# Kernel optimization log

Measured on AMD Instinct MI355X. Metric: run time of the kernel, lower is better.

Reference implementation:

```python
import jax, jax.numpy as jnp
import numpy as np

N = 50000      # nodes
E = 800000     # edges (avg degree 16)
D_IN, D_H, D_OUT = 128, 256, 128


def setup_inputs() -> dict:
    key = jax.random.key(0)
    ks = jax.random.split(key, 12)
    x = jax.random.normal(ks[0], (N, D_IN), jnp.float32)
    src = jax.random.randint(ks[1], (E,), 0, N)
    dst = jax.random.randint(ks[2], (E,), 0, N)

    def lin(k, din, dout):
        return (jax.random.normal(k, (din, dout), jnp.float32) / np.sqrt(din)).astype(jnp.float32)

    dims = [(D_IN, D_H), (D_H, D_H), (D_H, D_OUT)]
    params = {}
    ki = 3
    for i, (di, do) in enumerate(dims):
        params[f"W_self{i}"] = lin(ks[ki], di, do); ki += 1
        params[f"W_neigh{i}"] = lin(ks[ki], di, do); ki += 1
        params[f"b{i}"] = jnp.zeros((do,), jnp.float32)
    return {"x": x, "src": src, "dst": dst, **params}


def _mean_agg(h, src, dst):
    # gather src features along edges, segment-mean into dst nodes
    msg = jnp.take(h, src, axis=0)                              # [E, D]
    s = jax.ops.segment_sum(msg, dst, num_segments=N)           # [N, D]
    deg = jax.ops.segment_sum(jnp.ones((dst.shape[0], 1), h.dtype), dst, num_segments=N)
    return s / jnp.maximum(deg, 1.0)                            # zero-degree -> 0, as in DGL


def reference(x, src, dst,
              W_self0, W_neigh0, b0,
              W_self1, W_neigh1, b1,
              W_self2, W_neigh2, b2):
    Ws = [(W_self0, W_neigh0, b0), (W_self1, W_neigh1, b1), (W_self2, W_neigh2, b2)]
    h = x
    for i, (Ws_i, Wn_i, b_i) in enumerate(Ws):
        neigh = _mean_agg(h, src, dst)
        h = h @ Ws_i + neigh @ Wn_i + b_i                       # SAGEConv('mean')
        if i < len(Ws) - 1:
            h = jax.nn.relu(h)                                  # activation between layers
    return h
```

## Files before the change

### kernel.cpp

```cpp
#include <hip/hip_runtime.h>

#define NN 50000
#define NE 800000
#define NCHK 200
#define CHKE 4000
#define NBUK 196
#define BCAP 5120
#define NOFF (NBUK * NCHK)
#define NSB  ((NOFF + 255) / 256)

typedef __attribute__((ext_vector_type(8))) short short8;
typedef __attribute__((ext_vector_type(4))) float f32x4;
typedef unsigned int u32;
typedef unsigned short u16;

__device__ __forceinline__ float bf2f(short u) {
    union { unsigned int i; float f; } c;
    c.i = ((unsigned int)(unsigned short)u) << 16;
    return c.f;
}
__device__ __forceinline__ short f2bf(float f) {
    union { float f; unsigned int i; } c; c.f = f;
    unsigned int u = c.i;
    unsigned int r = (u + 0x7FFFu + ((u >> 16) & 1u)) >> 16;
    return (short)r;
}


__global__ void cvt_f32_bf16_kernel(const float* __restrict__ in, short* __restrict__ out, int n) {
    int gid = blockIdx.x * 256 + threadIdx.x;
    if (gid < n) out[gid] = f2bf(in[gid]);
}

__global__ void wcvt_all_kernel(const float* __restrict__ Ws0, const float* __restrict__ Wn0,
                                const float* __restrict__ Ws1, const float* __restrict__ Wn1,
                                const float* __restrict__ Ws2, const float* __restrict__ Wn2,
                                short* __restrict__ wts) {
    int gid = blockIdx.x * 256 + threadIdx.x;
    const float* W; int K, Dout, base, loc;
    if (gid < 65536)       { K = 128; Dout = 256; base = (gid < 32768)  ? 0 : 32768;
                             W = (gid < 32768)  ? Ws0 : Wn0; loc = gid & 32767; }
    else if (gid < 196608) { K = 256; Dout = 256; base = (gid < 131072) ? 65536 : 131072;
                             W = (gid < 131072) ? Ws1 : Wn1; loc = (gid - 65536) & 65535; }
    else                   { K = 256; Dout = 128; base = (gid < 229376) ? 196608 : 229376;
                             W = (gid < 229376) ? Ws2 : Wn2; loc = (gid - 196608) & 32767; }
    int k = loc / Dout, d = loc - k * Dout;
    int kt = k >> 6, ks = (k >> 5) & 1, kg = (k >> 3) & 3, j = k & 7;
    int cgp = d >> 4, l = d & 15;
    int off = ((((kt * 2 + ks) * (Dout >> 4) + cgp) * 4 + kg) * 16 + l) * 8 + j;
    wts[base + off] = f2bf(W[(long)k * Dout + d]);
}

__global__ __launch_bounds__(256) void bucket_hist_kernel(const int* __restrict__ dst,
                                                          int* __restrict__ chist) {
    __shared__ int lh[NBUK];
    int b = blockIdx.x, t = threadIdx.x;
    for (int i = t; i < NBUK; i += 256) lh[i] = 0;
    __syncthreads();
    int base = b * CHKE;
    for (int i = t; i < CHKE; i += 256) atomicAdd(&lh[dst[base + i] >> 8], 1);
    __syncthreads();
    for (int i = t; i < NBUK; i += 256) chist[i * NCHK + b] = lh[i];
}

__global__ __launch_bounds__(256) void off_blocksum_kernel(const int* __restrict__ in,
                                                           int* __restrict__ bsum) {
    __shared__ int sm[256];
    int t = threadIdx.x;
    int idx = blockIdx.x * 256 + t;
    sm[t] = (idx < NOFF) ? in[idx] : 0;
    __syncthreads();
    for (int off = 128; off > 0; off >>= 1) {
        if (t < off) sm[t] += sm[t + off];
        __syncthreads();
    }
    if (t == 0) bsum[blockIdx.x] = sm[0];
}

__global__ __launch_bounds__(256) void off_scanb_kernel(const int* __restrict__ bsum,
                                                        int* __restrict__ bpre) {
    __shared__ int sm[256];
    int t = threadIdx.x;
    sm[t] = (t < NSB) ? bsum[t] : 0;
    __syncthreads();
    for (int o = 1; o < 256; o <<= 1) {
        int v = sm[t];
        int a = (t >= o) ? sm[t - o] : 0;
        __syncthreads();
        sm[t] = v + a;
        __syncthreads();
    }
    if (t < NSB) bpre[t] = (t == 0) ? 0 : sm[t - 1];
}

__global__ __launch_bounds__(256) void off_scatter_kernel(const int* __restrict__ in,
                                                          const int* __restrict__ bpre,
                                                          int* __restrict__ off) {
    __shared__ int sm[256];
    int t = threadIdx.x;
    int idx = blockIdx.x * 256 + t;
    int val = (idx < NOFF) ? in[idx] : 0;
    sm[t] = val;
    __syncthreads();
    for (int o = 1; o < 256; o <<= 1) {
        int v = sm[t];
        int a = (t >= o) ? sm[t - o] : 0;
        __syncthreads();
        sm[t] = v + a;
        __syncthreads();
    }
    if (idx < NOFF) off[idx] = bpre[blockIdx.x] + sm[t] - val;
}

__global__ __launch_bounds__(256) void bucket_scatter_kernel(const int* __restrict__ src,
                                                             const int* __restrict__ dst,
                                                             const int* __restrict__ off,
                                                             u32* __restrict__ ebuf) {
    __shared__ int lcur[NBUK];
    int b = blockIdx.x, t = threadIdx.x;
    for (int i = t; i < NBUK; i += 256) lcur[i] = off[i * NCHK + b];
    __syncthreads();
    int base = b * CHKE;
    for (int i = t; i < CHKE; i += 256) {
        int d = dst[base + i], s = src[base + i];
        int slot = atomicAdd(&lcur[d >> 8], 1);
        ebuf[slot] = ((u32)(d & 255) << 16) | (u32)s;
    }
}

__global__ __launch_bounds__(256) void bucket_sort_kernel(const u32* __restrict__ ebuf,
                                                          const int* __restrict__ off,
                                                          u16* __restrict__ srcs16,
                                                          int* __restrict__ row_start,
                                                          int* __restrict__ cnt) {
    __shared__ u32 earr[BCAP];
    __shared__ u16 s16[BCAP];
    __shared__ int lhist[256], lpre[256], lcur[256];
    int k = blockIdx.x, t = threadIdx.x;
    int base = off[k * NCHK];
    int end  = (k < NBUK - 1) ? off[(k + 1) * NCHK] : NE;
    int nE = end - base;
    lhist[t] = 0;
    __syncthreads();
    for (int i = t; i < nE; i += 256) {
        u32 e = ebuf[base + i];
        earr[i] = e;
        atomicAdd(&lhist[e >> 16], 1);
    }
    __syncthreads();
    int v = lhist[t];
    lpre[t] = v;
    __syncthreads();
    for (int o = 1; o < 256; o <<= 1) {
        int x = lpre[t];
        int a = (t >= o) ? lpre[t - o] : 0;
        __syncthreads();
        lpre[t] = x + a;
        __syncthreads();
    }
    int excl = lpre[t] - v;
    int node = k * 256 + t;
    if (node < NN) { row_start[node] = base + excl; cnt[node] = v; }
    lcur[t] = excl;
    __syncthreads();
    for (int i = t; i < nE; i += 256) {
        u32 e = earr[i];
        int pos = atomicAdd(&lcur[e >> 16], 1);
        s16[pos] = (u16)(e & 0xFFFFu);
    }
    __syncthreads();
    for (int i = t; i < nE; i += 256) srcs16[base + i] = s16[i];
}

template<int NOUT, int KK, int GD, bool SAGE, bool RELU, bool OUT_F32>
__global__ __launch_bounds__(256, 4) void sage_fused_kernel(
    const short* __restrict__ A, const short* __restrict__ G,
    const short* __restrict__ Bs, const short* __restrict__ Bn,
    const float* __restrict__ bias, void* __restrict__ outp, int M,
    const u16* __restrict__ srcs, const int* __restrict__ row_start,
    const int* __restrict__ cnt, short* __restrict__ nb)
{
    constexpr int WN = NOUT / 64;
    constexpr int WM = 4 / WN;
    constexpr int MR = 64 / (WM * 16);
    constexpr int NR = 4;
    constexpr int KT = KK / 64;
    constexpr int NT = (SAGE ? 2 : 1) * KT;
    constexpr int CG = NOUT / 16;
    constexpr int CPR = GD / 8;
    constexpr int DPW = 64 / CPR;
    constexpr int GITERS = 16 / DPW;

    __shared__ short ldsA[2][64 * 64];

    const int tid  = threadIdx.x;
    const int wave = tid >> 6;
    const int lane = tid & 63;
    const int wm = wave / WN;
    const int wn = wave % WN;
    const int l15 = lane & 15;
    const int kg  = lane >> 4;
    const int bm  = blockIdx.x * 64;

    const int srow = tid >> 3;
    const int scol = ((tid & 7) << 3) ^ ((srow & 7) << 3);

    auto stage = [&](const short* __restrict__ Ap, int buf, int kt) {
        #pragma unroll
        for (int c = 0; c < 2; ++c) {
            const short* gp = Ap + (size_t)(bm + c * 32 + srow) * KK + kt * 64 + scol;
            __builtin_amdgcn_global_load_lds(
                (const __attribute__((address_space(1))) u32*)gp,
                (__attribute__((address_space(3))) u32*)(&ldsA[buf][c * 2048 + (wave << 9)]),
                16, 0, 0);
        }
    };

    stage(A, 0, 0);

    {
        const int sub = lane / CPR;
        const int cgi = lane % CPR;
        const short8* hp = (const short8*)G;
        #pragma unroll
        for (int it = 0; it < GITERS; ++it) {
            int v = bm + it * (4 * DPW) + wave * DPW + sub;
            if (v < NN) {
                const int c  = cnt[v];
                const int rs = row_start[v];
                float ac[8];
                #pragma unroll
                for (int j = 0; j < 8; ++j) ac[j] = 0.f;
                int i = 0;
                for (; i + 3 < c; i += 4) {
                    int s0 = srcs[rs + i], s1 = srcs[rs + i + 1];
                    int s2 = srcs[rs + i + 2], s3 = srcs[rs + i + 3];
                    short8 r0 = hp[(size_t)s0 * CPR + cgi];
                    short8 r1 = hp[(size_t)s1 * CPR + cgi];
                    short8 r2 = hp[(size_t)s2 * CPR + cgi];
                    short8 r3 = hp[(size_t)s3 * CPR + cgi];
                    #pragma unroll
                    for (int j = 0; j < 8; ++j)
                        ac[j] += (bf2f(r0[j]) + bf2f(r1[j])) + (bf2f(r2[j]) + bf2f(r3[j]));
                }
                for (; i < c; ++i) {
                    short8 r0 = hp[(size_t)srcs[rs + i] * CPR + cgi];
                    #pragma unroll
                    for (int j = 0; j < 8; ++j) ac[j] += bf2f(r0[j]);
                }
                float inv = (c > 0) ? (1.0f / (float)c) : 0.0f;
                short8 outv;
                #pragma unroll
                for (int j = 0; j < 8; ++j) outv[j] = f2bf(ac[j] * inv);
                ((short8*)nb)[(size_t)v * CPR + cgi] = outv;
            }
        }
    }
    __syncthreads();

    f32x4 acc[MR][NR];
    #pragma unroll
    for (int a = 0; a < MR; ++a)
        #pragma unroll
        for (int b = 0; b < NR; ++b)
            acc[a][b] = (f32x4){0.f, 0.f, 0.f, 0.f};

    for (int t = 0; t < NT; ++t) {
        const int cur = t & 1;
        if (t + 1 < NT) {
            const int np = (t + 1) / KT, nk = (t + 1) - np * KT;
            stage(np ? nb : A, cur ^ 1, nk);
        }
        const int ph = t / KT, kt = t - ph * KT;
        const short* __restrict__ Wb = ph ? Bn : Bs;

        #pragma unroll
        for (int ks = 0; ks < 2; ++ks) {
            short8 wreg[NR];
            #pragma unroll
            for (int nr = 0; nr < NR; ++nr)
                wreg[nr] = *(const short8*)(
                    Wb + (size_t)((((kt * 2 + ks) * CG + wn * NR + nr) * 4 + kg) * 16 + l15) * 8);
            short8 areg[MR];
            #pragma unroll
            for (int mr = 0; mr < MR; ++mr) {
                int r = wm * (MR * 16) + mr * 16 + l15;
                areg[mr] = *(const short8*)(&ldsA[cur][r * 64 + ((ks * 32 + kg * 8) ^ ((r & 7) << 3))]);
            }
            #pragma unroll
            for (int mr = 0; mr < MR; ++mr)
                #pragma unroll
                for (int nr = 0; nr < NR; ++nr)
                    acc[mr][nr] = __builtin_amdgcn_mfma_f32_16x16x32_bf16(
                        areg[mr], wreg[nr], acc[mr][nr], 0, 0, 0);
        }
        __syncthreads();
    }

    #pragma unroll
    for (int mr = 0; mr < MR; ++mr) {
        int rowb = bm + wm * (MR * 16) + mr * 16 + kg * 4;
        #pragma unroll
        for (int nr = 0; nr < NR; ++nr) {
            int col = wn * 64 + nr * 16 + l15;
            float bv = bias ? bias[col] : 0.f;
            #pragma unroll
            for (int r = 0; r < 4; ++r) {
                int row = rowb + r;
                if (row < M) {
                    float vv = acc[mr][nr][r] + bv;
                    if (!SAGE) vv += bf2f(nb[(size_t)row * NOUT + col]);
                    if (RELU) vv = fmaxf(vv, 0.f);
                    if (OUT_F32) ((float*)outp)[(size_t)row * NOUT + col] = vv;
                    else         ((short*)outp)[(size_t)row * NOUT + col] = f2bf(vv);
                }
            }
        }
    }
}

template<int NOUT, int KK, int PHASES, bool RELU, bool OUT_F32, bool ADDIN, bool BIAS>
__global__ __launch_bounds__(256, 4) void gemm_sage5_kernel(
    const short* __restrict__ Aself, const short* __restrict__ Aneigh,
    const short* __restrict__ Bself, const short* __restrict__ Bneigh,
    const float* __restrict__ bias, void* __restrict__ outp, int M,
    const short* __restrict__ addin)
{
    constexpr int WN = NOUT / 64;
    constexpr int WM = 4 / WN;
    constexpr int BM = 64 * WM;
    constexpr int SC = BM / 32;
    constexpr int MR = 4;
    constexpr int NR = 4;
    constexpr int KT = KK / 64;
    constexpr int NT = PHASES * KT;
    constexpr int CG = NOUT / 16;

    __shared__ short ldsA[2][BM * 64];

    const int tid  = threadIdx.x;
    const int wave = tid >> 6;
    const int lane = tid & 63;
    const int wm = wave / WN;
    const int wn = wave % WN;
    const int l15 = lane & 15;
    const int kg  = lane >> 4;
    const int bm  = blockIdx.x * BM;

    f32x4 acc[MR][NR];
    #pragma unroll
    for (int a = 0; a < MR; ++a)
        #pragma unroll
        for (int b = 0; b < NR; ++b)
            acc[a][b] = (f32x4){0.f, 0.f, 0.f, 0.f};

    const int srow = tid >> 3;
    const int scol = ((tid & 7) << 3) ^ ((srow & 7) << 3);

    auto stageA = [&](int buf, int t) {
        int ph = t / KT, kt = t - ph * KT;
        const short* A = ph ? Aneigh : Aself;
        #pragma unroll
        for (int c = 0; c < SC; ++c) {
            const short* gp = A + (size_t)(bm + c * 32 + srow) * KK + kt * 64 + scol;
            __builtin_amdgcn_global_load_lds(
                (const __attribute__((address_space(1))) u32*)gp,
                (__attribute__((address_space(3))) u32*)(&ldsA[buf][c * 2048 + (wave << 9)]),
                16, 0, 0);
        }
    };

    stageA(0, 0);
    __syncthreads();

    for (int t = 0; t < NT; ++t) {
        const int cur = t & 1;
        if (t + 1 < NT) stageA(cur ^ 1, t + 1);
        const int ph = t / KT, kt = t - ph * KT;
        const short* __restrict__ Wb = ph ? Bneigh : Bself;

        #pragma unroll
        for (int ks = 0; ks < 2; ++ks) {
            short8 wreg[NR];
            #pragma unroll
            for (int nr = 0; nr < NR; ++nr)
                wreg[nr] = *(const short8*)(
                    Wb + (size_t)((((kt * 2 + ks) * CG + wn * NR + nr) * 4 + kg) * 16 + l15) * 8);
            short8 areg[MR];
            #pragma unroll
            for (int mr = 0; mr < MR; ++mr) {
                int r = wm * 64 + mr * 16 + l15;
                areg[mr] = *(const short8*)(&ldsA[cur][r * 64 + ((ks * 32 + kg * 8) ^ ((r & 7) << 3))]);
            }
            #pragma unroll
            for (int mr = 0; mr < MR; ++mr)
                #pragma unroll
                for (int nr = 0; nr < NR; ++nr)
                    acc[mr][nr] = __builtin_amdgcn_mfma_f32_16x16x32_bf16(
                        areg[mr], wreg[nr], acc[mr][nr], 0, 0, 0);
        }
        __syncthreads();
    }

    #pragma unroll
    for (int mr = 0; mr < MR; ++mr) {
        int rowb = bm + wm * 64 + mr * 16 + kg * 4;
        #pragma unroll
        for (int nr = 0; nr < NR; ++nr) {
            int col = wn * 64 + nr * 16 + l15;
            float bv = BIAS ? bias[col] : 0.f;
            #pragma unroll
            for (int r = 0; r < 4; ++r) {
                int row = rowb + r;
                if (row < M) {
                    float vv = acc[mr][nr][r] + bv;
                    if (ADDIN) vv += bf2f(addin[(size_t)row * NOUT + col]);
                    if (RELU) vv = fmaxf(vv, 0.f);
                    if (OUT_F32) ((float*)outp)[(size_t)row * NOUT + col] = vv;
                    else         ((short*)outp)[(size_t)row * NOUT + col] = f2bf(vv);
                }
            }
        }
    }
}


extern "C" void kernel_launch(void* const* d_in, const int* in_sizes, int n_in,
                              void* d_out, int out_size, void* d_ws, size_t ws_size,
                              hipStream_t stream) {
    const float* x    = (const float*)d_in[0];
    const int*   srcp = (const int*)d_in[1];
    const int*   dstp = (const int*)d_in[2];
    const float* Ws0  = (const float*)d_in[3];
    const float* Wn0  = (const float*)d_in[4];
    const float* b0   = (const float*)d_in[5];
    const float* Ws1  = (const float*)d_in[6];
    const float* Wn1  = (const float*)d_in[7];
    const float* b1   = (const float*)d_in[8];
    const float* Ws2  = (const float*)d_in[9];
    const float* Wn2  = (const float*)d_in[10];
    const float* b2   = (const float*)d_in[11];

    char* base = (char*)d_ws;
    size_t off_b = 0;
    auto alloc = [&](size_t bytes) -> void* {
        void* p = base + off_b;
        off_b += (bytes + 255) & ~(size_t)255;
        return p;
    };

    int*   cnt       = (int*)alloc((size_t)NN * 4);
    int*   row_start = (int*)alloc((size_t)NN * 4);
    int*   chist     = (int*)alloc((size_t)NOFF * 4);
    int*   offb      = (int*)alloc((size_t)NOFF * 4);
    int*   bsum      = (int*)alloc((size_t)NSB * 4);
    int*   bpre      = (int*)alloc((size_t)NSB * 4);
    u32*   ebuf      = (u32*)alloc((size_t)NE * 4);
    u16*   srcs16    = (u16*)alloc((size_t)NE * 2);
    short* hA        = (short*)alloc((size_t)NN * 256 * 2);
    short* hB        = (short*)alloc((size_t)NN * 256 * 2);
    short* nb        = (short*)alloc((size_t)NN * 256 * 2);
    short* wts       = (short*)alloc((size_t)262144 * 2 + 131072);
    short* Wt0s = wts;
    short* Wt0n = Wt0s + 32768;
    short* Wt1s = Wt0n + 32768;
    short* Wt1n = Wt1s + 65536;
    short* Wt2s = Wt1n + 65536;
    short* Wt2n = Wt2s + 32768;

    bucket_hist_kernel<<<NCHK, 256, 0, stream>>>(dstp, chist);
    off_blocksum_kernel<<<NSB, 256, 0, stream>>>(chist, bsum);
    off_scanb_kernel<<<1, 256, 0, stream>>>(bsum, bpre);
    off_scatter_kernel<<<NSB, 256, 0, stream>>>(chist, bpre, offb);
    bucket_scatter_kernel<<<NCHK, 256, 0, stream>>>(srcp, dstp, offb, ebuf);
    bucket_sort_kernel<<<NBUK, 256, 0, stream>>>(ebuf, offb, srcs16, row_start, cnt);

    wcvt_all_kernel<<<1024, 256, 0, stream>>>(Ws0, Wn0, Ws1, Wn1, Ws2, Wn2, wts);

    cvt_f32_bf16_kernel<<<(NN * 128 + 255) / 256, 256, 0, stream>>>(x, hA, NN * 128);

    const int fblk    = (NN + 63) / 64;
    const int mblk128 = (NN + 127) / 128;

    sage_fused_kernel<256, 128, 128, true, true, false><<<fblk, 256, 0, stream>>>(
        hA, hA, Wt0s, Wt0n, b0, hB, NN, srcs16, row_start, cnt, nb);

    sage_fused_kernel<256, 256, 256, true, true, false><<<fblk, 256, 0, stream>>>(
        hB, hB, Wt1s, Wt1n, b1, hA, NN, srcs16, row_start, cnt, nb);

    gemm_sage5_kernel<128, 256, 1, false, false, false, false><<<mblk128, 256, 0, stream>>>(
        hA, hA, Wt2n, Wt2n, nullptr, hB, NN, nullptr);
    sage_fused_kernel<128, 256, 128, false, false, true><<<fblk, 256, 0, stream>>>(
        hA, hB, Wt2s, Wt2s, b2, d_out, NN, srcs16, row_start, cnt, nb);
}
```

Before: 241.3 us.

## Split fused SAGE kernel into gather and MFMA wave groups, keep aggregates in LDS

Each block now has 512 threads. Four waves gather and average neighbour features straight into swizzled LDS. The other four waves compute the self GEMM at the same time, loading A fragments directly from global memory, then finish the neighbour GEMM from LDS after a barrier. This removes the global round trip of the neighbour buffer and overlaps the gather latency with self-GEMM MFMA work. In exchange it uses more LDS per block and loses the staged LDS reuse for the self operand, which may lower occupancy.

```diff
diff --git a/kernel.cpp b/kernel.cpp
--- a/kernel.cpp
+++ b/kernel.cpp
@@ -173,58 +173,46 @@
 }
 
 template<int NOUT, int KK, int GD, bool SAGE, bool RELU, bool OUT_F32>
-__global__ __launch_bounds__(256, 4) void sage_fused_kernel(
+__global__ __launch_bounds__(512, 2) void sage_pc_kernel(
     const short* __restrict__ A, const short* __restrict__ G,
     const short* __restrict__ Bs, const short* __restrict__ Bn,
     const float* __restrict__ bias, void* __restrict__ outp, int M,
     const u16* __restrict__ srcs, const int* __restrict__ row_start,
-    const int* __restrict__ cnt, short* __restrict__ nb)
+    const int* __restrict__ cnt)
 {
-    constexpr int WN = NOUT / 64;
-    constexpr int WM = 4 / WN;
-    constexpr int MR = 64 / (WM * 16);
-    constexpr int NR = 4;
+    constexpr int GT = GD / 64;
     constexpr int KT = KK / 64;
-    constexpr int NT = (SAGE ? 2 : 1) * KT;
     constexpr int CG = NOUT / 16;
     constexpr int CPR = GD / 8;
     constexpr int DPW = 64 / CPR;
     constexpr int GITERS = 16 / DPW;
-
-    __shared__ short ldsA[2][64 * 64];
+    constexpr int CWN = (NOUT == 256) ? 4 : 2;
+    constexpr int MR = (NOUT == 256) ? 4 : 2;
+    constexpr int NR = 4;
+
+    __shared__ short lds_n[GT * 4096];
 
     const int tid  = threadIdx.x;
     const int wave = tid >> 6;
     const int lane = tid & 63;
-    const int wm = wave / WN;
-    const int wn = wave % WN;
+    const int bm   = blockIdx.x * 64;
     const int l15 = lane & 15;
     const int kg  = lane >> 4;
-    const int bm  = blockIdx.x * 64;
-
-    const int srow = tid >> 3;
-    const int scol = ((tid & 7) << 3) ^ ((srow & 7) << 3);
-
-    auto stage = [&](const short* __restrict__ Ap, int buf, int kt) {
-        #pragma unroll
-        for (int c = 0; c < 2; ++c) {
-            const short* gp = Ap + (size_t)(bm + c * 32 + srow) * KK + kt * 64 + scol;
-            __builtin_amdgcn_global_load_lds(
-                (const __attribute__((address_space(1))) u32*)gp,
-                (__attribute__((address_space(3))) u32*)(&ldsA[buf][c * 2048 + (wave << 9)]),
-                16, 0, 0);
-        }
-    };
-
-    stage(A, 0, 0);
-
-    {
+    const int wv  = wave - 4;
+    const int wn  = (NOUT == 256) ? wv : (wv & 1);
+    const int wm  = (NOUT == 256) ? 0 : (wv >> 1);
+
+    f32x4 acc[MR][NR];
+
+    if (wave < 4) {
         const int sub = lane / CPR;
         const int cgi = lane % CPR;
+        const int kt  = cgi >> 3;
+        const int kw  = (cgi & 7) * 8;
         const short8* hp = (const short8*)G;
-        #pragma unroll
         for (int it = 0; it < GITERS; ++it) {
-            int v = bm + it * (4 * DPW) + wave * DPW + sub;
+            int r = wave * 16 + it * DPW + sub;
+            int v = bm + r;
             if (v < NN) {
                 const int c  = cnt[v];
                 const int rs = row_start[v];
@@ -233,7 +221,7 @@
                 for (int j = 0; j < 8; ++j) ac[j] = 0.f;
                 int i = 0;
                 for (; i + 3 < c; i += 4) {
-                    int s0 = srcs[rs + i], s1 = srcs[rs + i + 1];
+                    int s0 = srcs[rs + i],     s1 = srcs[rs + i + 1];
                     int s2 = srcs[rs + i + 2], s3 = srcs[rs + i + 3];
                     short8 r0 = hp[(size_t)s0 * CPR + cgi];
                     short8 r1 = hp[(size_t)s1 * CPR + cgi];
@@ -252,67 +240,89 @@
                 short8 outv;
                 #pragma unroll
                 for (int j = 0; j < 8; ++j) outv[j] = f2bf(ac[j] * inv);
-                ((short8*)nb)[(size_t)v * CPR + cgi] = outv;
+                *(short8*)(&lds_n[kt * 4096 + r * 64 + (kw ^ ((r & 7) << 3))]) = outv;
             }
         }
-    }
-    __syncthreads();
-
-    f32x4 acc[MR][NR];
-    #pragma unroll
-    for (int a = 0; a < MR; ++a)
+    } else {
         #pragma unroll
-        for (int b = 0; b < NR; ++b)
-            acc[a][b] = (f32x4){0.f, 0.f, 0.f, 0.f};
-
-    for (int t = 0; t < NT; ++t) {
-        const int cur = t & 1;
-        if (t + 1 < NT) {
-            const int np = (t + 1) / KT, nk = (t + 1) - np * KT;
-            stage(np ? nb : A, cur ^ 1, nk);
-        }
-        const int ph = t / KT, kt = t - ph * KT;
-        const short* __restrict__ Wb = ph ? Bn : Bs;
-
+        for (int a = 0; a < MR; ++a)
+            #pragma unroll
+            for (int b = 0; b < NR; ++b)
+                acc[a][b] = (f32x4){0.f, 0.f, 0.f, 0.f};
+        for (int kt = 0; kt < KT; ++kt) {
+            #pragma unroll
+            for (int ks = 0; ks < 2; ++ks) {
+                short8 wreg[NR];
+                #pragma unroll
+                for (int nr = 0; nr < NR; ++nr)
+                    wreg[nr] = *(const short8*)(
+                        Bs + (size_t)((((kt * 2 + ks) * CG + wn * NR + nr) * 4 + kg) * 16 + l15) * 8);
+                short8 areg[MR];
+                #pragma unroll
+                for (int mr = 0; mr < MR; ++mr) {
+                    int row = bm + wm * (MR * 16) + mr * 16 + l15;
+                    areg[mr] = *(const short8*)(A + (size_t)row * KK + kt * 64 + ks * 32 + kg * 8);
+                }
+                #pragma unroll
+                for (int mr = 0; mr < MR; ++mr)
+                    #pragma unroll
+                    for (int nr = 0; nr < NR; ++nr)
+                        acc[mr][nr] = __builtin_amdgcn_mfma_f32_16x16x32_bf16(
+                            areg[mr], wreg[nr], acc[mr][nr], 0, 0, 0);
+            }
+        }
+    }
+
+    __syncthreads();
+
+    if (wave >= 4) {
+        if constexpr (SAGE) {
+            for (int kt = 0; kt < GT; ++kt) {
+                #pragma unroll
+                for (int ks = 0; ks < 2; ++ks) {
+                    short8 wreg[NR];
+                    #pragma unroll
+                    for (int nr = 0; nr < NR; ++nr)
+                        wreg[nr] = *(const short8*)(
+                            Bn + (size_t)((((kt * 2 + ks) * CG + wn * NR + nr) * 4 + kg) * 16 + l15) * 8);
+                    short8 areg[MR];
+                    #pragma unroll
+                    for (int mr = 0; mr < MR; ++mr) {
+                        int r = wm * (MR * 16) + mr * 16 + l15;
+                        areg[mr] = *(const short8*)(
+                            &lds_n[kt * 4096 + r * 64 + ((ks * 32 + kg * 8) ^ ((r & 7) << 3))]);
+                    }
+                    #pragma unroll
+                    for (int mr = 0; mr < MR; ++mr)
+                        #pragma unroll
+                        for (int nr = 0; nr < NR; ++nr)
+                            acc[mr][nr] = __builtin_amdgcn_mfma_f32_16x16x32_bf16(
+                                areg[mr], wreg[nr], acc[mr][nr], 0, 0, 0);
+                }
+            }
+        }
         #pragma unroll
-        for (int ks = 0; ks < 2; ++ks) {
-            short8 wreg[NR];
-            #pragma unroll
-            for (int nr = 0; nr < NR; ++nr)
-                wreg[nr] = *(const short8*)(
-                    Wb + (size_t)((((kt * 2 + ks) * CG + wn * NR + nr) * 4 + kg) * 16 + l15) * 8);
-            short8 areg[MR];
-            #pragma unroll
-            for (int mr = 0; mr < MR; ++mr) {
-                int r = wm * (MR * 16) + mr * 16 + l15;
-                areg[mr] = *(const short8*)(&ldsA[cur][r * 64 + ((ks * 32 + kg * 8) ^ ((r & 7) << 3))]);
-            }
-            #pragma unroll
-            for (int mr = 0; mr < MR; ++mr)
-                #pragma unroll
-                for (int nr = 0; nr < NR; ++nr)
-                    acc[mr][nr] = __builtin_amdgcn_mfma_f32_16x16x32_bf16(
-                        areg[mr], wreg[nr], acc[mr][nr], 0, 0, 0);
-        }
-        __syncthreads();
-    }
-
-    #pragma unroll
-    for (int mr = 0; mr < MR; ++mr) {
-        int rowb = bm + wm * (MR * 16) + mr * 16 + kg * 4;
-        #pragma unroll
-        for (int nr = 0; nr < NR; ++nr) {
-            int col = wn * 64 + nr * 16 + l15;
-            float bv = bias ? bias[col] : 0.f;
-            #pragma unroll
-            for (int r = 0; r < 4; ++r) {
-                int row = rowb + r;
-                if (row < M) {
-                    float vv = acc[mr][nr][r] + bv;
-                    if (!SAGE) vv += bf2f(nb[(size_t)row * NOUT + col]);
-                    if (RELU) vv = fmaxf(vv, 0.f);
-                    if (OUT_F32) ((float*)outp)[(size_t)row * NOUT + col] = vv;
-                    else         ((short*)outp)[(size_t)row * NOUT + col] = f2bf(vv);
+        for (int mr = 0; mr < MR; ++mr) {
+            int rowb = bm + wm * (MR * 16) + mr * 16 + kg * 4;
+            #pragma unroll
+            for (int nr = 0; nr < NR; ++nr) {
+                int col = wn * 64 + nr * 16 + l15;
+                float bv = bias ? bias[col] : 0.f;
+                #pragma unroll
+                for (int r = 0; r < 4; ++r) {
+                    int row = rowb + r;
+                    if (row < M) {
+                        float vv = acc[mr][nr][r] + bv;
+                        if (!SAGE) {
+                            int rl = row - bm;
+                            int kt = col >> 6, g7 = (col >> 3) & 7, j = col & 7;
+                            vv += bf2f(lds_n[kt * 4096 + rl * 64 +
+                                             ((g7 * 8) ^ ((rl & 7) << 3)) + j]);
+                        }
+                        if (RELU) vv = fmaxf(vv, 0.f);
+                        if (OUT_F32) ((float*)outp)[(size_t)row * NOUT + col] = vv;
+                        else         ((short*)outp)[(size_t)row * NOUT + col] = f2bf(vv);
+                    }
                 }
             }
         }
@@ -459,7 +469,6 @@
     u16*   srcs16    = (u16*)alloc((size_t)NE * 2);
     short* hA        = (short*)alloc((size_t)NN * 256 * 2);
     short* hB        = (short*)alloc((size_t)NN * 256 * 2);
-    short* nb        = (short*)alloc((size_t)NN * 256 * 2);
     short* wts       = (short*)alloc((size_t)262144 * 2 + 131072);
     short* Wt0s = wts;
     short* Wt0n = Wt0s + 32768;
@@ -482,14 +491,14 @@
     const int fblk    = (NN + 63) / 64;
     const int mblk128 = (NN + 127) / 128;
 
-    sage_fused_kernel<256, 128, 128, true, true, false><<<fblk, 256, 0, stream>>>(
-        hA, hA, Wt0s, Wt0n, b0, hB, NN, srcs16, row_start, cnt, nb);
-
-    sage_fused_kernel<256, 256, 256, true, true, false><<<fblk, 256, 0, stream>>>(
-        hB, hB, Wt1s, Wt1n, b1, hA, NN, srcs16, row_start, cnt, nb);
+    sage_pc_kernel<256, 128, 128, true, true, false><<<fblk, 512, 0, stream>>>(
+        hA, hA, Wt0s, Wt0n, b0, hB, NN, srcs16, row_start, cnt);
+
+    sage_pc_kernel<256, 256, 256, true, true, false><<<fblk, 512, 0, stream>>>(
+        hB, hB, Wt1s, Wt1n, b1, hA, NN, srcs16, row_start, cnt);
 
     gemm_sage5_kernel<128, 256, 1, false, false, false, false><<<mblk128, 256, 0, stream>>>(
         hA, hA, Wt2n, Wt2n, nullptr, hB, NN, nullptr);
-    sage_fused_kernel<128, 256, 128, false, false, true><<<fblk, 256, 0, stream>>>(
-        hA, hB, Wt2s, Wt2s, b2, d_out, NN, srcs16, row_start, cnt, nb);
-}
+    sage_pc_kernel<128, 256, 128, false, false, true><<<fblk, 512, 0, stream>>>(
+        hA, hB, Wt2s, Wt2n, b2, d_out, NN, srcs16, row_start, cnt);
+}
```

Measured after the change: 388.7 us. 1.61x slower.
